# Performance work log

Measured on AMD Instinct MI355X. Metric: run time of the kernel, lower is better.

## Reference

```python
import jax, jax.numpy as jnp
import numpy as np

HEAD_NUMS = 8
LN_EPS = 1e-5


def _layernorm(x, g, b):
    m = jnp.mean(x, axis=-1, keepdims=True)
    v = jnp.var(x, axis=-1, keepdims=True)
    return (x - m) * jax.lax.rsqrt(v + LN_EPS) * g + b


def setup_inputs() -> dict:
    key = jax.random.key(0)
    ks = jax.random.split(key, 6)
    B, S, D = 4, 2048, 512
    x = jax.random.normal(ks[0], (B, S, D), dtype=jnp.float32)
    W1 = jax.random.normal(ks[1], (4 * D, D), dtype=jnp.float32) * 0.02
    b1 = jnp.zeros((4 * D,), dtype=jnp.float32)
    ln_g = jnp.ones((D,), dtype=jnp.float32)
    ln_b = jnp.zeros((D,), dtype=jnp.float32)
    W2 = jax.random.normal(ks[2], (D, D), dtype=jnp.float32) * 0.02
    b2 = jnp.zeros((D,), dtype=jnp.float32)
    return {"x": x, "W1": W1, "b1": b1, "ln_g": ln_g, "ln_b": ln_b, "W2": W2, "b2": b2}


def reference(x, W1, b1, ln_g, ln_b, W2, b2):
    B, S, D = x.shape
    H = HEAD_NUMS
    hd = D // H
    # fused qkv+gate projection with SiLU (HSTU style)
    h = jax.nn.silu(x @ W1.T + b1)                   # [B,S,4D]
    h = h.reshape(B, S, 4, H, hd)                    # split into gate,q,k,v
    gate = jnp.transpose(h[:, :, 0], (0, 2, 1, 3))   # [B,H,S,hd]
    q = jnp.transpose(h[:, :, 1], (0, 2, 1, 3))
    k = jnp.transpose(h[:, :, 2], (0, 2, 1, 3))
    v = jnp.transpose(h[:, :, 3], (0, 2, 1, 3))
    scale = 1.0 / np.sqrt(hd).astype(np.float32)
    scores = jnp.einsum('bhsd,bhtd->bhst', q, k) * scale   # [B,H,S,S]
    causal = jnp.tril(jnp.ones((S, S), dtype=bool))        # allowed: t <= s
    # silu replaces softmax; masked (future) positions contribute 0
    # (mathematical limit of silu(-inf) is 0)
    a = jnp.where(causal, jax.nn.silu(scores), 0.0)
    o = jnp.einsum('bhst,bhtd->bhsd', a, v)                # [B,H,S,hd]
    o = jnp.transpose(o, (0, 2, 1, 3)).reshape(B, S, D)
    normed = _layernorm(o, ln_g, ln_b)
    gate_f = jnp.transpose(gate, (0, 2, 1, 3)).reshape(B, S, D)
    return (normed * gate_f) @ W2.T + b2
```

## Files before the change

kernel.cpp:

```cpp
#include <hip/hip_runtime.h>
#include <hip/hip_bf16.h>
#include <cstdint>


typedef __attribute__((ext_vector_type(8))) short short8;
typedef __attribute__((ext_vector_type(4))) float f32x4;

__device__ __forceinline__ unsigned short f2bf(float f) {
  union { float f; unsigned u; } v; v.f = f;
  unsigned r = v.u + 0x7FFFu + ((v.u >> 16) & 1u);
  return (unsigned short)(r >> 16);
}
__device__ __forceinline__ float bf2f(unsigned short h) {
  union { unsigned u; float f; } v; v.u = ((unsigned)h) << 16; return v.f;
}
__device__ __forceinline__ float fast_rcp(float x) {
#if __has_builtin(__builtin_amdgcn_rcpf)
  return __builtin_amdgcn_rcpf(x);
#else
  return 1.0f / x;
#endif
}
__device__ __forceinline__ float fast_exp2(float x) {
#if __has_builtin(__builtin_amdgcn_exp2f)
  return __builtin_amdgcn_exp2f(x);
#else
  return exp2f(x);
#endif
}
__device__ __forceinline__ float silu_f(float x) {
  return x * fast_rcp(1.0f + fast_exp2(-1.442695041f * x));
}
__device__ __forceinline__ unsigned pk2(float lo, float hi) {
  union { __hip_bfloat162 b; unsigned u; } cv;
  cv.b = __float22bfloat162_rn(make_float2(lo, hi));
  return cv.u;
}
__device__ __forceinline__ void gl_lds16(const void* g, void* l) {
  __builtin_amdgcn_global_load_lds(
      (const __attribute__((address_space(1))) void*)g,
      (__attribute__((address_space(3))) void*)l, 16, 0, 0);
}

__global__ void convert_kernel(const float* __restrict__ x, const float* __restrict__ w1,
                               const float* __restrict__ w2,
                               unsigned short* __restrict__ xb, unsigned short* __restrict__ w1b,
                               unsigned short* __restrict__ w2b) {
  int i = blockIdx.x * 256 + threadIdx.x;
  const float* s; unsigned short* d;
  if (i < 1048576) { s = x; d = xb; }
  else if (i < 1048576 + 262144) { i -= 1048576; s = w1; d = w1b; }
  else { i -= (1048576 + 262144); if (i >= 65536) return; s = w2; d = w2b; }
  float4 f = ((const float4*)s)[i];
  uint2 o; o.x = pk2(f.x, f.y); o.y = pk2(f.z, f.w);
  ((uint2*)d)[i] = o;
}

__global__ __launch_bounds__(256, 3) void gemm1_kernel(
    const unsigned short* __restrict__ xb,
    const unsigned short* __restrict__ w1b,
    const float* __restrict__ b1,
    unsigned short* __restrict__ h,
    unsigned short* __restrict__ vt)
{
  __shared__ __align__(16) unsigned short smem[16896];
  unsigned short* As = smem;
  unsigned short* Bs = smem + 8192;
  const int tid = threadIdx.x;
  const int w = tid >> 6, l = tid & 63;
  const int bm = blockIdx.x & 63, bn = blockIdx.x >> 6;
  const int wm = w & 1, wn = w >> 1;
  const int quad = l >> 4, lc = l & 15, lc7 = lc & 7;
  const int r8 = l >> 3, c8 = (l & 7) ^ r8;

  f32x4 acc[4][4] = {};
  const unsigned short* ga = xb + (size_t)(bm * 128 + w * 32 + r8) * 512 + c8 * 8;
  const unsigned short* gb = w1b + (size_t)(bn * 128 + w * 32 + r8) * 512 + c8 * 8;

  for (int kt = 0; kt < 512; kt += 64) {
#pragma unroll
    for (int i = 0; i < 4; ++i) {
      gl_lds16(ga + i * 8 * 512 + kt, As + (w * 4 + i) * 512);
      gl_lds16(gb + i * 8 * 512 + kt, Bs + (w * 4 + i) * 512);
    }
    __syncthreads();
#pragma unroll
    for (int kk = 0; kk < 2; ++kk) {
      short8 af[4], bf[4];
#pragma unroll
      for (int mt = 0; mt < 4; ++mt)
        af[mt] = *(const short8*)(As + (wm * 64 + mt * 16 + lc) * 64 +
                                  (((kk * 4 + quad) ^ lc7) * 8));
#pragma unroll
      for (int nt = 0; nt < 4; ++nt)
        bf[nt] = *(const short8*)(Bs + (wn * 64 + nt * 16 + lc) * 64 +
                                  (((kk * 4 + quad) ^ lc7) * 8));
#pragma unroll
      for (int mt = 0; mt < 4; ++mt)
#pragma unroll
        for (int nt = 0; nt < 4; ++nt)
          acc[mt][nt] = __builtin_amdgcn_mfma_f32_16x16x32_bf16(af[mt], bf[nt], acc[mt][nt], 0, 0, 0);
    }
    __syncthreads();
  }

  unsigned short* T = smem;
  const int sec = bn >> 2;
  if (sec == 3) {
#pragma unroll
    for (int nt = 0; nt < 4; ++nt) {
      const int nl = wn * 64 + nt * 16 + lc;
      const float bias = b1[bn * 128 + nl];
#pragma unroll
      for (int mt = 0; mt < 4; ++mt) {
        const int sl = wm * 64 + mt * 16 + quad * 4;
        uint2 pk;
        pk.x = pk2(silu_f(acc[mt][nt][0] + bias), silu_f(acc[mt][nt][1] + bias));
        pk.y = pk2(silu_f(acc[mt][nt][2] + bias), silu_f(acc[mt][nt][3] + bias));
        *(uint2*)(T + nl * 132 + sl) = pk;
      }
    }
  } else {
    const float osc = (sec == 1) ? 0.125f : 1.0f;
#pragma unroll
    for (int nt = 0; nt < 4; ++nt) {
      const int nl = wn * 64 + nt * 16 + lc;
      const float bias = b1[bn * 128 + nl];
#pragma unroll
      for (int mt = 0; mt < 4; ++mt) {
        const int sl = wm * 64 + mt * 16 + quad * 4;
#pragma unroll
        for (int r = 0; r < 4; ++r)
          T[(sl + r) * 132 + nl] = f2bf(silu_f(acc[mt][nt][r] + bias) * osc);
      }
    }
  }
  __syncthreads();
  const int rrow = tid >> 4, rcol = (tid & 15) * 8;
  if (sec == 3) {
    const int bq = bm >> 4, sbase = (bm & 15) * 128;
#pragma unroll
    for (int p = 0; p < 8; ++p) {
      const int row = p * 16 + rrow;
      const int n = bn * 128 + row, hh = (n >> 6) & 7, d = n & 63;
      *(short8*)(vt + (size_t)((bq * 8 + hh) * 64 + d) * 2048 + sbase + rcol) =
          *(const short8*)(T + row * 132 + rcol);
    }
  } else {
#pragma unroll
    for (int p = 0; p < 8; ++p) {
      const int row = p * 16 + rrow;
      *(short8*)(h + (size_t)(bm * 128 + row) * 2048 + bn * 128 + rcol) =
          *(const short8*)(T + row * 132 + rcol);
    }
  }
}

__global__ __launch_bounds__(256, 3) void attn_kernel(
    const unsigned short* __restrict__ h,
    const unsigned short* __restrict__ vt,
    float* __restrict__ o)
{
  __shared__ __align__(16) unsigned short smem[17408];
  unsigned short* Ks = smem;
  unsigned short* Vs = smem + 8192;
  const int tid = threadIdx.x;
  const int w = tid >> 6, l = tid & 63;
  const int bh = blockIdx.x & 31;
  const int qi = 31 - (blockIdx.x >> 5);
  const int b = bh >> 3, hh = bh & 7;
  const int quad = l >> 4, lc = l & 15, lc7 = lc & 7;
  const int r8 = l >> 3, c8 = (l & 7) ^ r8;
  const int wm = w & 1, wn = w >> 1;
  const int q0 = qi * 64;
  const int nk = (qi >> 1) + 1;
  const int addrA = (((quad & 1) * 2) * 16 + lc) * 4;
  const int addrB = addrA + 64;
  const bool hiq = (quad >> 1) != 0;

  {
    const unsigned short* qg =
        h + (size_t)(b * 2048 + q0 + w * 16 + r8) * 2048 + 512 + hh * 64 + c8 * 8;
#pragma unroll
    for (int i = 0; i < 2; ++i)
      gl_lds16(qg + (size_t)i * 8 * 2048, Ks + (w * 2 + i) * 512);
  }
  __syncthreads();
  short8 qf[2][2];
#pragma unroll
  for (int nt = 0; nt < 2; ++nt)
#pragma unroll
    for (int kk = 0; kk < 2; ++kk)
      qf[nt][kk] = *(const short8*)(Ks + (wn * 32 + nt * 16 + lc) * 64 +
                                    (((kk * 4 + quad) ^ lc7) * 8));

  f32x4 oacc[2][4] = {};

  const unsigned short* kg =
      h + (size_t)(b * 2048 + w * 32 + r8) * 2048 + 1024 + hh * 64 + c8 * 8;
  const int vrow = l >> 4, vcol = l & 15;
  const unsigned short* vgE =
      vt + (size_t)(bh * 64 + w * 16 + vrow) * 2048 + ((vcol ^ vrow) * 8);
  const unsigned short* vgO =
      vt + (size_t)(bh * 64 + w * 16 + vrow) * 2048 + ((vcol ^ vrow ^ 4) * 8);

  for (int ti = 0; ti < nk; ++ti) {
    __syncthreads();
    const int toff = ti * 128;
#pragma unroll
    for (int i = 0; i < 4; ++i) {
      gl_lds16(kg + (size_t)(toff + i * 8) * 2048, Ks + (w * 4 + i) * 512);
      const unsigned short* vsrc = ((i & 1) ? vgO : vgE) + (size_t)(i * 4) * 2048 + toff;
      gl_lds16(vsrc, Vs + (w * 4 + i) * 512);
    }
    __syncthreads();

    f32x4 sc[4][2] = {};
#pragma unroll
    for (int kk = 0; kk < 2; ++kk) {
      short8 kf[4];
#pragma unroll
      for (int mt = 0; mt < 4; ++mt)
        kf[mt] = *(const short8*)(Ks + (wm * 64 + mt * 16 + lc) * 64 +
                                  (((kk * 4 + quad) ^ lc7) * 8));
#pragma unroll
      for (int mt = 0; mt < 4; ++mt)
#pragma unroll
        for (int nt = 0; nt < 2; ++nt)
          sc[mt][nt] = __builtin_amdgcn_mfma_f32_16x16x32_bf16(kf[mt], qf[nt][kk], sc[mt][nt], 0, 0, 0);
    }

    unsigned pd[4][2][2];
    if (ti < nk - 1) {
#pragma unroll
      for (int mt = 0; mt < 4; ++mt)
#pragma unroll
        for (int nt = 0; nt < 2; ++nt) {
          pd[mt][nt][0] = pk2(silu_f(sc[mt][nt][0]), silu_f(sc[mt][nt][1]));
          pd[mt][nt][1] = pk2(silu_f(sc[mt][nt][2]), silu_f(sc[mt][nt][3]));
        }
    } else {
#pragma unroll
      for (int mt = 0; mt < 4; ++mt) {
        const int tg = toff + wm * 64 + mt * 16 + quad * 4;
#pragma unroll
        for (int nt = 0; nt < 2; ++nt) {
          const int qg = q0 + wn * 32 + nt * 16 + lc;
          float v0 = (tg + 0 <= qg) ? silu_f(sc[mt][nt][0]) : 0.0f;
          float v1 = (tg + 1 <= qg) ? silu_f(sc[mt][nt][1]) : 0.0f;
          float v2 = (tg + 2 <= qg) ? silu_f(sc[mt][nt][2]) : 0.0f;
          float v3 = (tg + 3 <= qg) ? silu_f(sc[mt][nt][3]) : 0.0f;
          pd[mt][nt][0] = pk2(v0, v1);
          pd[mt][nt][1] = pk2(v2, v3);
        }
      }
    }

#pragma unroll
    for (int c = 0; c < 2; ++c) {
      short8 vf[4];
#pragma unroll
      for (int dt = 0; dt < 4; ++dt)
        vf[dt] = *(const short8*)(Vs + (dt * 16 + lc) * 128 +
                                  (((wm * 8 + c * 4 + quad) ^ lc7) * 8));
#pragma unroll
      for (int nt = 0; nt < 2; ++nt) {
        int lo0 = __builtin_amdgcn_ds_bpermute(addrA, (int)pd[2 * c][nt][0]);
        int hi0 = __builtin_amdgcn_ds_bpermute(addrA, (int)pd[2 * c + 1][nt][0]);
        int lo1 = __builtin_amdgcn_ds_bpermute(addrA, (int)pd[2 * c][nt][1]);
        int hi1 = __builtin_amdgcn_ds_bpermute(addrA, (int)pd[2 * c + 1][nt][1]);
        int lo2 = __builtin_amdgcn_ds_bpermute(addrB, (int)pd[2 * c][nt][0]);
        int hi2 = __builtin_amdgcn_ds_bpermute(addrB, (int)pd[2 * c + 1][nt][0]);
        int lo3 = __builtin_amdgcn_ds_bpermute(addrB, (int)pd[2 * c][nt][1]);
        int hi3 = __builtin_amdgcn_ds_bpermute(addrB, (int)pd[2 * c + 1][nt][1]);
        int4 pfu;
        pfu.x = hiq ? hi0 : lo0;
        pfu.y = hiq ? hi1 : lo1;
        pfu.z = hiq ? hi2 : lo2;
        pfu.w = hiq ? hi3 : lo3;
        short8 pf = *(short8*)&pfu;
#pragma unroll
        for (int dt = 0; dt < 4; ++dt)
          oacc[nt][dt] = __builtin_amdgcn_mfma_f32_16x16x32_bf16(pf, vf[dt], oacc[nt][dt], 0, 0, 0);
      }
    }
  }

  __syncthreads();
  float* R = (float*)smem;
  if (wm == 1) {
#pragma unroll
    for (int nt = 0; nt < 2; ++nt)
#pragma unroll
      for (int dt = 0; dt < 4; ++dt)
        *(f32x4*)(R + (dt * 16 + lc) * 68 + wn * 32 + nt * 16 + quad * 4) = oacc[nt][dt];
  }
  __syncthreads();
  if (wm == 0) {
    float* og = o + (size_t)(b * 2048 + q0 + wn * 32) * 512 + hh * 64;
#pragma unroll
    for (int nt = 0; nt < 2; ++nt)
#pragma unroll
      for (int dt = 0; dt < 4; ++dt) {
        f32x4 rr = *(const f32x4*)(R + (dt * 16 + lc) * 68 + wn * 32 + nt * 16 + quad * 4);
        f32x4 v = oacc[nt][dt];
        v[0] += rr[0]; v[1] += rr[1]; v[2] += rr[2]; v[3] += rr[3];
#pragma unroll
        for (int r = 0; r < 4; ++r)
          og[(nt * 16 + quad * 4 + r) * 512 + dt * 16 + lc] = v[r];
      }
  }
}

__global__ __launch_bounds__(256) void ln_gate_kernel(
    const float* __restrict__ o, const unsigned short* __restrict__ h,
    const float* __restrict__ lng, const float* __restrict__ lnb,
    unsigned short* __restrict__ y) {
  const int row = blockIdx.x * 4 + (threadIdx.x >> 6);
  const int l = threadIdx.x & 63;
  const float4* orow = (const float4*)(o + (size_t)row * 512);
  float4 a = orow[l * 2], c = orow[l * 2 + 1];
  float s0 = a.x + a.y + a.z + a.w + c.x + c.y + c.z + c.w;
#pragma unroll
  for (int off = 32; off > 0; off >>= 1) s0 += __shfl_xor(s0, off);
  const float mean = s0 * (1.0f / 512.0f);
  float dx[8] = {a.x - mean, a.y - mean, a.z - mean, a.w - mean,
                 c.x - mean, c.y - mean, c.z - mean, c.w - mean};
  float sq = 0.f;
#pragma unroll
  for (int j = 0; j < 8; ++j) sq += dx[j] * dx[j];
#pragma unroll
  for (int off = 32; off > 0; off >>= 1) sq += __shfl_xor(sq, off);
  const float inv = rsqrtf(sq * (1.0f / 512.0f) + 1e-5f);
  const float4* g4 = (const float4*)lng;
  const float4* b4 = (const float4*)lnb;
  float4 g0 = g4[l * 2], g1 = g4[l * 2 + 1], bb0 = b4[l * 2], bb1 = b4[l * 2 + 1];
  const unsigned short* grow = h + (size_t)row * 2048;
  ushort4 gr0 = *(const ushort4*)(grow + l * 8);
  ushort4 gr1 = *(const ushort4*)(grow + l * 8 + 4);
  float gg[8] = {g0.x, g0.y, g0.z, g0.w, g1.x, g1.y, g1.z, g1.w};
  float bbv[8] = {bb0.x, bb0.y, bb0.z, bb0.w, bb1.x, bb1.y, bb1.z, bb1.w};
  float gv[8] = {bf2f(gr0.x), bf2f(gr0.y), bf2f(gr0.z), bf2f(gr0.w),
                 bf2f(gr1.x), bf2f(gr1.y), bf2f(gr1.z), bf2f(gr1.w)};
  float r[8];
#pragma unroll
  for (int j = 0; j < 8; ++j) r[j] = (dx[j] * inv * gg[j] + bbv[j]) * gv[j];
  uint2 p0, p1;
  p0.x = pk2(r[0], r[1]); p0.y = pk2(r[2], r[3]);
  p1.x = pk2(r[4], r[5]); p1.y = pk2(r[6], r[7]);
  uint2* yrow = (uint2*)(y + (size_t)row * 512);
  yrow[l * 2] = p0;
  yrow[l * 2 + 1] = p1;
}

__global__ __launch_bounds__(256, 3) void gemm2_kernel(
    const unsigned short* __restrict__ yb,
    const unsigned short* __restrict__ w2b,
    const float* __restrict__ b2, float* __restrict__ out) {
  __shared__ __align__(16) unsigned short As[64 * 64];
  __shared__ __align__(16) unsigned short Bs[64 * 64];
  const int tid = threadIdx.x;
  const int w = tid >> 6, l = tid & 63;
  const int bm = blockIdx.x & 127, bn = blockIdx.x >> 7;
  const int wm = w & 1, wn = w >> 1;
  const int quad = l >> 4, lc = l & 15, lc7 = lc & 7;
  const int r8 = l >> 3, c8 = (l & 7) ^ r8;

  f32x4 acc[2][2] = {};
  const unsigned short* ga = yb + (size_t)(bm * 64 + w * 16 + r8) * 512 + c8 * 8;
  const unsigned short* gb = w2b + (size_t)(bn * 64 + w * 16 + r8) * 512 + c8 * 8;

  for (int kt = 0; kt < 512; kt += 64) {
#pragma unroll
    for (int j = 0; j < 2; ++j) {
      gl_lds16(ga + j * 8 * 512 + kt, As + (w * 2 + j) * 512);
      gl_lds16(gb + j * 8 * 512 + kt, Bs + (w * 2 + j) * 512);
    }
    __syncthreads();
#pragma unroll
    for (int kk = 0; kk < 2; ++kk) {
      short8 af[2], bf[2];
#pragma unroll
      for (int mt = 0; mt < 2; ++mt)
        af[mt] = *(const short8*)(As + (wm * 32 + mt * 16 + lc) * 64 +
                                  (((kk * 4 + quad) ^ lc7) * 8));
#pragma unroll
      for (int nt = 0; nt < 2; ++nt)
        bf[nt] = *(const short8*)(Bs + (wn * 32 + nt * 16 + lc) * 64 +
                                  (((kk * 4 + quad) ^ lc7) * 8));
#pragma unroll
      for (int mt = 0; mt < 2; ++mt)
#pragma unroll
        for (int nt = 0; nt < 2; ++nt)
          acc[mt][nt] = __builtin_amdgcn_mfma_f32_16x16x32_bf16(af[mt], bf[nt], acc[mt][nt], 0, 0, 0);
    }
    __syncthreads();
  }

#pragma unroll
  for (int nt = 0; nt < 2; ++nt) {
    const int n = bn * 64 + wn * 32 + nt * 16 + lc;
    const float bias = b2[n];
#pragma unroll
    for (int mt = 0; mt < 2; ++mt) {
      const int m0 = bm * 64 + wm * 32 + mt * 16 + quad * 4;
#pragma unroll
      for (int r = 0; r < 4; ++r)
        out[(size_t)(m0 + r) * 512 + n] = acc[mt][nt][r] + bias;
    }
  }
}

extern "C" void kernel_launch(void* const* d_in, const int* in_sizes, int n_in,
                              void* d_out, int out_size, void* d_ws, size_t ws_size,
                              hipStream_t stream) {
  const float* x = (const float*)d_in[0];
  const float* W1 = (const float*)d_in[1];
  const float* b1 = (const float*)d_in[2];
  const float* lng = (const float*)d_in[3];
  const float* lnb = (const float*)d_in[4];
  const float* W2 = (const float*)d_in[5];
  const float* b2 = (const float*)d_in[6];
  float* out = (float*)d_out;
  char* ws = (char*)d_ws;

  unsigned short* xb  = (unsigned short*)(ws);
  unsigned short* w1b = (unsigned short*)(ws + 8388608);
  unsigned short* w2b = (unsigned short*)(ws + 10485760);
  unsigned short* h   = (unsigned short*)(ws + 11010048);
  unsigned short* vt  = (unsigned short*)(ws + 44564480);
  float* o            = (float*)(ws + 52953088);
  unsigned short* yb  = (unsigned short*)(ws + 69730304);

  convert_kernel<<<5376, 256, 0, stream>>>(x, W1, W2, xb, w1b, w2b);
  gemm1_kernel<<<1024, 256, 0, stream>>>(xb, w1b, b1, h, vt);
  attn_kernel<<<1024, 256, 0, stream>>>(h, vt, o);
  ln_gate_kernel<<<2048, 256, 0, stream>>>(o, h, lng, lnb, yb);
  gemm2_kernel<<<1024, 256, 0, stream>>>(yb, w2b, b2, out);
}
```

Measured before the change: 165.3 us.

## Restructure causal attention into 64-key tiles with LDS-staged P and folded scaling

The attention kernel moves from 128-key tiles, where two warp groups split keys and reduce partial outputs at the end, to 64-key tiles where each warp owns 16 query rows. SiLU scores go through a padded LDS buffer instead of ds_bpermute shuffles, which drops the final cross-warp reduction and the masked waste in the last half-tile. The log2(e) factor is folded into the q scale so SiLU uses a bare exp2. The resulting constant output scale is absorbed by LayerNorm, with epsilon rescaled to match. Occupancy is raised to 5 blocks per CU, at the cost of twice as many tile iterations and barriers per block.

Measured after the change: 159.8 us. 1.03x faster.

```diff
diff --git a/kernel.cpp b/kernel.cpp
--- a/kernel.cpp
+++ b/kernel.cpp
@@ -30,6 +30,9 @@
 }
 __device__ __forceinline__ float silu_f(float x) {
   return x * fast_rcp(1.0f + fast_exp2(-1.442695041f * x));
+}
+__device__ __forceinline__ float psilu(float s) {
+  return s * fast_rcp(1.0f + fast_exp2(-s));
 }
 __device__ __forceinline__ unsigned pk2(float lo, float hi) {
   union { __hip_bfloat162 b; unsigned u; } cv;
@@ -121,7 +124,7 @@
       }
     }
   } else {
-    const float osc = (sec == 1) ? 0.125f : 1.0f;
+    const float osc = (sec == 1) ? 0.18033688f : 1.0f;
 #pragma unroll
     for (int nt = 0; nt < 4; ++nt) {
       const int nl = wn * 64 + nt * 16 + lc;
@@ -156,34 +159,30 @@
   }
 }
 
-__global__ __launch_bounds__(256, 3) void attn_kernel(
+__global__ __launch_bounds__(256, 5) void attn_kernel(
     const unsigned short* __restrict__ h,
     const unsigned short* __restrict__ vt,
     float* __restrict__ o)
 {
-  __shared__ __align__(16) unsigned short smem[17408];
-  unsigned short* Ks = smem;
-  unsigned short* Vs = smem + 8192;
+  __shared__ __align__(16) unsigned short Ks[64 * 64];
+  __shared__ __align__(16) unsigned short Vs[64 * 64];
+  __shared__ __align__(16) unsigned short Ps[64 * 72];
   const int tid = threadIdx.x;
   const int w = tid >> 6, l = tid & 63;
   const int bh = blockIdx.x & 31;
   const int qi = 31 - (blockIdx.x >> 5);
   const int b = bh >> 3, hh = bh & 7;
   const int quad = l >> 4, lc = l & 15, lc7 = lc & 7;
-  const int r8 = l >> 3, c8 = (l & 7) ^ r8;
+  const int r8 = l >> 3, c8 = (l & 7) ^ (r8 & 7);
   const int wm = w & 1, wn = w >> 1;
   const int q0 = qi * 64;
-  const int nk = (qi >> 1) + 1;
-  const int addrA = (((quad & 1) * 2) * 16 + lc) * 4;
-  const int addrB = addrA + 64;
-  const bool hiq = (quad >> 1) != 0;
+  const int nk = qi + 1;
 
   {
     const unsigned short* qg =
         h + (size_t)(b * 2048 + q0 + w * 16 + r8) * 2048 + 512 + hh * 64 + c8 * 8;
-#pragma unroll
-    for (int i = 0; i < 2; ++i)
-      gl_lds16(qg + (size_t)i * 8 * 2048, Ks + (w * 2 + i) * 512);
+    gl_lds16(qg, Ks + (w * 16) * 64);
+    gl_lds16(qg + (size_t)8 * 2048, Ks + (w * 16 + 8) * 64);
   }
   __syncthreads();
   short8 qf[2][2];
@@ -194,122 +193,85 @@
       qf[nt][kk] = *(const short8*)(Ks + (wn * 32 + nt * 16 + lc) * 64 +
                                     (((kk * 4 + quad) ^ lc7) * 8));
 
-  f32x4 oacc[2][4] = {};
+  f32x4 oacc[4] = {};
 
   const unsigned short* kg =
-      h + (size_t)(b * 2048 + w * 32 + r8) * 2048 + 1024 + hh * 64 + c8 * 8;
-  const int vrow = l >> 4, vcol = l & 15;
-  const unsigned short* vgE =
-      vt + (size_t)(bh * 64 + w * 16 + vrow) * 2048 + ((vcol ^ vrow) * 8);
-  const unsigned short* vgO =
-      vt + (size_t)(bh * 64 + w * 16 + vrow) * 2048 + ((vcol ^ vrow ^ 4) * 8);
+      h + (size_t)(b * 2048 + w * 16 + r8) * 2048 + 1024 + hh * 64 + c8 * 8;
+  const unsigned short* vg = vt + (size_t)(bh * 64 + w * 16 + r8) * 2048 + c8 * 8;
 
   for (int ti = 0; ti < nk; ++ti) {
     __syncthreads();
-    const int toff = ti * 128;
-#pragma unroll
-    for (int i = 0; i < 4; ++i) {
-      gl_lds16(kg + (size_t)(toff + i * 8) * 2048, Ks + (w * 4 + i) * 512);
-      const unsigned short* vsrc = ((i & 1) ? vgO : vgE) + (size_t)(i * 4) * 2048 + toff;
-      gl_lds16(vsrc, Vs + (w * 4 + i) * 512);
-    }
-    __syncthreads();
-
-    f32x4 sc[4][2] = {};
+    const int toff = ti * 64;
+    gl_lds16(kg + (size_t)toff * 2048, Ks + (w * 16) * 64);
+    gl_lds16(kg + (size_t)(toff + 8) * 2048, Ks + (w * 16 + 8) * 64);
+    gl_lds16(vg + toff, Vs + (w * 16) * 64);
+    gl_lds16(vg + (size_t)8 * 2048 + toff, Vs + (w * 16 + 8) * 64);
+    __syncthreads();
+
+    f32x4 sc[2][2] = {};
 #pragma unroll
     for (int kk = 0; kk < 2; ++kk) {
-      short8 kf[4];
-#pragma unroll
-      for (int mt = 0; mt < 4; ++mt)
-        kf[mt] = *(const short8*)(Ks + (wm * 64 + mt * 16 + lc) * 64 +
+      short8 kf[2];
+#pragma unroll
+      for (int mt = 0; mt < 2; ++mt)
+        kf[mt] = *(const short8*)(Ks + (wm * 32 + mt * 16 + lc) * 64 +
                                   (((kk * 4 + quad) ^ lc7) * 8));
 #pragma unroll
-      for (int mt = 0; mt < 4; ++mt)
+      for (int mt = 0; mt < 2; ++mt)
 #pragma unroll
         for (int nt = 0; nt < 2; ++nt)
           sc[mt][nt] = __builtin_amdgcn_mfma_f32_16x16x32_bf16(kf[mt], qf[nt][kk], sc[mt][nt], 0, 0, 0);
     }
 
-    unsigned pd[4][2][2];
     if (ti < nk - 1) {
 #pragma unroll
-      for (int mt = 0; mt < 4; ++mt)
+      for (int mt = 0; mt < 2; ++mt) {
+        const int tloc = wm * 32 + mt * 16 + quad * 4;
 #pragma unroll
         for (int nt = 0; nt < 2; ++nt) {
-          pd[mt][nt][0] = pk2(silu_f(sc[mt][nt][0]), silu_f(sc[mt][nt][1]));
-          pd[mt][nt][1] = pk2(silu_f(sc[mt][nt][2]), silu_f(sc[mt][nt][3]));
-        }
-    } else {
-#pragma unroll
-      for (int mt = 0; mt < 4; ++mt) {
-        const int tg = toff + wm * 64 + mt * 16 + quad * 4;
-#pragma unroll
-        for (int nt = 0; nt < 2; ++nt) {
-          const int qg = q0 + wn * 32 + nt * 16 + lc;
-          float v0 = (tg + 0 <= qg) ? silu_f(sc[mt][nt][0]) : 0.0f;
-          float v1 = (tg + 1 <= qg) ? silu_f(sc[mt][nt][1]) : 0.0f;
-          float v2 = (tg + 2 <= qg) ? silu_f(sc[mt][nt][2]) : 0.0f;
-          float v3 = (tg + 3 <= qg) ? silu_f(sc[mt][nt][3]) : 0.0f;
-          pd[mt][nt][0] = pk2(v0, v1);
-          pd[mt][nt][1] = pk2(v2, v3);
+          const int qloc = wn * 32 + nt * 16 + lc;
+          uint2 pk;
+          pk.x = pk2(psilu(sc[mt][nt][0]), psilu(sc[mt][nt][1]));
+          pk.y = pk2(psilu(sc[mt][nt][2]), psilu(sc[mt][nt][3]));
+          *(uint2*)(Ps + qloc * 72 + tloc) = pk;
         }
       }
-    }
-
-#pragma unroll
-    for (int c = 0; c < 2; ++c) {
-      short8 vf[4];
-#pragma unroll
-      for (int dt = 0; dt < 4; ++dt)
-        vf[dt] = *(const short8*)(Vs + (dt * 16 + lc) * 128 +
-                                  (((wm * 8 + c * 4 + quad) ^ lc7) * 8));
-#pragma unroll
-      for (int nt = 0; nt < 2; ++nt) {
-        int lo0 = __builtin_amdgcn_ds_bpermute(addrA, (int)pd[2 * c][nt][0]);
-        int hi0 = __builtin_amdgcn_ds_bpermute(addrA, (int)pd[2 * c + 1][nt][0]);
-        int lo1 = __builtin_amdgcn_ds_bpermute(addrA, (int)pd[2 * c][nt][1]);
-        int hi1 = __builtin_amdgcn_ds_bpermute(addrA, (int)pd[2 * c + 1][nt][1]);
-        int lo2 = __builtin_amdgcn_ds_bpermute(addrB, (int)pd[2 * c][nt][0]);
-        int hi2 = __builtin_amdgcn_ds_bpermute(addrB, (int)pd[2 * c + 1][nt][0]);
-        int lo3 = __builtin_amdgcn_ds_bpermute(addrB, (int)pd[2 * c][nt][1]);
-        int hi3 = __builtin_amdgcn_ds_bpermute(addrB, (int)pd[2 * c + 1][nt][1]);
-        int4 pfu;
-        pfu.x = hiq ? hi0 : lo0;
-        pfu.y = hiq ? hi1 : lo1;
-        pfu.z = hiq ? hi2 : lo2;
-        pfu.w = hiq ? hi3 : lo3;
-        short8 pf = *(short8*)&pfu;
-#pragma unroll
-        for (int dt = 0; dt < 4; ++dt)
-          oacc[nt][dt] = __builtin_amdgcn_mfma_f32_16x16x32_bf16(pf, vf[dt], oacc[nt][dt], 0, 0, 0);
+    } else {
+#pragma unroll
+      for (int mt = 0; mt < 2; ++mt) {
+        const int tloc = wm * 32 + mt * 16 + quad * 4;
+#pragma unroll
+        for (int nt = 0; nt < 2; ++nt) {
+          const int qloc = wn * 32 + nt * 16 + lc;
+          float v0 = (tloc + 0 <= qloc) ? psilu(sc[mt][nt][0]) : 0.0f;
+          float v1 = (tloc + 1 <= qloc) ? psilu(sc[mt][nt][1]) : 0.0f;
+          float v2 = (tloc + 2 <= qloc) ? psilu(sc[mt][nt][2]) : 0.0f;
+          float v3 = (tloc + 3 <= qloc) ? psilu(sc[mt][nt][3]) : 0.0f;
+          uint2 pk; pk.x = pk2(v0, v1); pk.y = pk2(v2, v3);
+          *(uint2*)(Ps + qloc * 72 + tloc) = pk;
+        }
       }
     }
-  }
-
-  __syncthreads();
-  float* R = (float*)smem;
-  if (wm == 1) {
-#pragma unroll
-    for (int nt = 0; nt < 2; ++nt)
-#pragma unroll
-      for (int dt = 0; dt < 4; ++dt)
-        *(f32x4*)(R + (dt * 16 + lc) * 68 + wn * 32 + nt * 16 + quad * 4) = oacc[nt][dt];
-  }
-  __syncthreads();
-  if (wm == 0) {
-    float* og = o + (size_t)(b * 2048 + q0 + wn * 32) * 512 + hh * 64;
-#pragma unroll
-    for (int nt = 0; nt < 2; ++nt)
+    __syncthreads();
+
+#pragma unroll
+    for (int ks = 0; ks < 2; ++ks) {
+      short8 pf = *(const short8*)(Ps + (w * 16 + lc) * 72 + ks * 32 + quad * 8);
 #pragma unroll
       for (int dt = 0; dt < 4; ++dt) {
-        f32x4 rr = *(const f32x4*)(R + (dt * 16 + lc) * 68 + wn * 32 + nt * 16 + quad * 4);
-        f32x4 v = oacc[nt][dt];
-        v[0] += rr[0]; v[1] += rr[1]; v[2] += rr[2]; v[3] += rr[3];
-#pragma unroll
-        for (int r = 0; r < 4; ++r)
-          og[(nt * 16 + quad * 4 + r) * 512 + dt * 16 + lc] = v[r];
+        short8 vf = *(const short8*)(Vs + (dt * 16 + lc) * 64 +
+                                     (((ks * 4 + quad) ^ lc7) * 8));
+        oacc[dt] = __builtin_amdgcn_mfma_f32_16x16x32_bf16(pf, vf, oacc[dt], 0, 0, 0);
       }
-  }
+    }
+  }
+
+  float* og = o + (size_t)(b * 2048 + q0 + w * 16) * 512 + hh * 64;
+#pragma unroll
+  for (int dt = 0; dt < 4; ++dt)
+#pragma unroll
+    for (int r = 0; r < 4; ++r)
+      og[(quad * 4 + r) * 512 + dt * 16 + lc] = oacc[dt][r];
 }
 
 __global__ __launch_bounds__(256) void ln_gate_kernel(
@@ -331,7 +293,7 @@
   for (int j = 0; j < 8; ++j) sq += dx[j] * dx[j];
 #pragma unroll
   for (int off = 32; off > 0; off >>= 1) sq += __shfl_xor(sq, off);
-  const float inv = rsqrtf(sq * (1.0f / 512.0f) + 1e-5f);
+  const float inv = rsqrtf(sq * (1.0f / 512.0f) + 2.0813690e-5f);
   const float4* g4 = (const float4*)lng;
   const float4* b4 = (const float4*)lnb;
   float4 g0 = g4[l * 2], g1 = g4[l * 2 + 1], bb0 = b4[l * 2], bb1 = b4[l * 2 + 1];
```
